# Kernel tuning notes

Hardware: AMD Instinct MI355X
Metric: run time of the kernel (lower is better)

Reference implementation:

```python
import jax, jax.numpy as jnp
import numpy as np

N, E = 40000, 640000
EMB, HID, H, TXT = 128, 128, 4, 384
C = HID // H  # per-head channels = 32


def _prelu(x, a):
    return jnp.where(x >= 0, x, a * x)


def _layernorm(x, g, b, eps=1e-5):
    m = jnp.mean(x, axis=-1, keepdims=True)
    v = jnp.mean((x - m) ** 2, axis=-1, keepdims=True)
    return (x - m) / jnp.sqrt(v + eps) * g + b


def _gat_conv(h, src, dst, W, att_src, att_dst, bias):
    # PyG GATConv (concat=True, eval mode): lin has no bias, self-loops already in src/dst.
    xh = (h @ W.T).reshape(N, H, C)                      # [N,H,C]
    a_src = jnp.sum(xh * att_src, axis=-1)               # [N,H]
    a_dst = jnp.sum(xh * att_dst, axis=-1)               # [N,H]
    alpha = jax.nn.leaky_relu(a_src[src] + a_dst[dst], negative_slope=0.2)  # [Et,H]
    amax = jax.ops.segment_max(alpha, dst, num_segments=N)
    ex = jnp.exp(alpha - amax[dst])
    denom = jax.ops.segment_sum(ex, dst, num_segments=N)
    coef = ex / denom[dst]                               # scatter-softmax over dst
    out = jax.ops.segment_sum(xh[src] * coef[:, :, None], dst, num_segments=N)
    return out.reshape(N, H * C) + bias


def setup_inputs() -> dict:
    key = jax.random.key(0)
    ks = jax.random.split(key, 20)
    nrm = lambda k, s, sc=0.05: jax.random.normal(k, s, jnp.float32) * sc
    inp = {
        "x": nrm(ks[0], (N, EMB), 1.0),
        "num_x": nrm(ks[1], (N, 1), 1.0),
        "num_mask": jnp.ones((N,), jnp.float32),
        "txt_x": nrm(ks[2], (N, TXT), 1.0),
        "txt_mask": jnp.ones((N,), jnp.float32),
        "edge_index": jax.random.randint(ks[3], (2, E), 0, N, jnp.int32),
        "num_proj_w": nrm(ks[4], (EMB, 1)), "num_proj_b": jnp.zeros((EMB,), jnp.float32),
        "txt_proj_w": nrm(ks[5], (EMB, TXT)), "txt_proj_b": jnp.zeros((EMB,), jnp.float32),
        "node_proj_w": nrm(ks[6], (HID, EMB)), "node_proj_b": jnp.zeros((HID,), jnp.float32),
        "prelu0_a": jnp.full((HID,), 0.25, jnp.float32),
        "conv1_w": nrm(ks[7], (HID, HID)), "att_src1": nrm(ks[8], (H, C)), "att_dst1": nrm(ks[9], (H, C)), "bias1": jnp.zeros((HID,), jnp.float32),
        "norm1_g": jnp.ones((HID,), jnp.float32), "norm1_b": jnp.zeros((HID,), jnp.float32),
        "prelu1_a": jnp.full((HID,), 0.25, jnp.float32),
        "conv2_w": nrm(ks[10], (HID, HID)), "att_src2": nrm(ks[11], (H, C)), "att_dst2": nrm(ks[12], (H, C)), "bias2": jnp.zeros((HID,), jnp.float32),
        "norm2_g": jnp.ones((HID,), jnp.float32), "norm2_b": jnp.zeros((HID,), jnp.float32),
        "prelu2_a": jnp.full((HID,), 0.25, jnp.float32),
        "out_w": nrm(ks[13], (1, HID)), "out_b": jnp.zeros((1,), jnp.float32),
    }
    return inp


def reference(x, num_x, num_mask, txt_x, txt_mask, edge_index,
              num_proj_w, num_proj_b, txt_proj_w, txt_proj_b,
              node_proj_w, node_proj_b, prelu0_a,
              conv1_w, att_src1, att_dst1, bias1, norm1_g, norm1_b, prelu1_a,
              conv2_w, att_src2, att_dst2, bias2, norm2_g, norm2_b, prelu2_a,
              out_w, out_b):
    # add self loops (PyG GATConv default)
    loop = jnp.arange(N, dtype=edge_index.dtype)
    src = jnp.concatenate([edge_index[0], loop])
    dst = jnp.concatenate([edge_index[1], loop])

    h = (num_x * num_mask[:, None]) @ num_proj_w.T + num_proj_b
    h = h + (txt_x * txt_mask[:, None]) @ txt_proj_w.T + txt_proj_b
    h = h + x @ node_proj_w.T + node_proj_b
    h = _prelu(h, prelu0_a)

    h = _gat_conv(h, src, dst, conv1_w, att_src1, att_dst1, bias1)
    h = _prelu(_layernorm(h, norm1_g, norm1_b), prelu1_a)  # dropout: eval mode -> identity

    h = _gat_conv(h, src, dst, conv2_w, att_src2, att_dst2, bias2)
    h = _prelu(_layernorm(h, norm2_g, norm2_b), prelu2_a)

    return (h @ out_w.T + out_b).squeeze(-1)  # [N]
```

## Files before the change

kernel.cpp:

```cpp
#include <hip/hip_runtime.h>
#include <stdint.h>

typedef unsigned short u16;
typedef unsigned int u32;
typedef __attribute__((ext_vector_type(8))) short bf16x8;
typedef __attribute__((ext_vector_type(4))) float f32x4;

__device__ __forceinline__ float bf2f(u32 u) {
    union { u32 i; float f; } v; v.i = u << 16; return v.f;
}
__device__ __forceinline__ u16 f2bf(float f) {
    u32 x = __float_as_uint(f);
    return (u16)((x + 0x7fffu + ((x >> 16) & 1u)) >> 16);
}
__device__ __forceinline__ float wred_sum(float v) {
#pragma unroll
    for (int o = 32; o > 0; o >>= 1) v += __shfl_xor(v, o, 64);
    return v;
}
__device__ __forceinline__ bf16x8 ldA_f32(const float* p, size_t off) {
    union { uint4 u; bf16x8 b; } t;
    const float* af = p + off;
    float4 a = *(const float4*)af, b2 = *(const float4*)(af + 4);
    t.u.x = (u32)f2bf(a.x)  | ((u32)f2bf(a.y)  << 16);
    t.u.y = (u32)f2bf(a.z)  | ((u32)f2bf(a.w)  << 16);
    t.u.z = (u32)f2bf(b2.x) | ((u32)f2bf(b2.y) << 16);
    t.u.w = (u32)f2bf(b2.z) | ((u32)f2bf(b2.w) << 16);
    return t.b;
}
__device__ __forceinline__ bf16x8 ld16B(const u16* p, size_t off) {
    union { uint4 u; bf16x8 b; } t; t.u = *(const uint4*)(p + off); return t.b;
}
__device__ __forceinline__ bf16x8 ldB(const u16* sw, int ct, int ks, int l16, int quad) {
    union { uint4 u; bf16x8 b; } t;
    t.u = *(const uint4*)&sw[(ct * 16 + l16) * 136 + ks * 32 + quad * 8];
    return t.b;
}
__device__ __forceinline__ void stage256_f32(const float* W, int stride, int koff,
                                             u16* sw, int tid) {
#pragma unroll
    for (int it = 0; it < 8; ++it) {
        int idx = (it * 256 + tid) * 8;
        int c = idx >> 7, kk = idx & 127;
        const float* wf = W + (size_t)c * stride + koff + kk;
        float4 a = *(const float4*)wf, b = *(const float4*)(wf + 4);
        uint4 v;
        v.x = (u32)f2bf(a.x) | ((u32)f2bf(a.y) << 16);
        v.y = (u32)f2bf(a.z) | ((u32)f2bf(a.w) << 16);
        v.z = (u32)f2bf(b.x) | ((u32)f2bf(b.y) << 16);
        v.w = (u32)f2bf(b.z) | ((u32)f2bf(b.w) << 16);
        *(uint4*)&sw[c * 136 + kk] = v;
    }
}

__global__ void k_zero(int* __restrict__ p, int n) {
    int i = blockIdx.x * 256 + threadIdx.x;
    if (i < n) p[i] = 0;
}
__global__ void k_hist(const int* __restrict__ dst, int E, int* __restrict__ deg) {
    int e = blockIdx.x * 256 + threadIdx.x;
    if (e < E) atomicAdd(&deg[dst[e]], 1);
}
__global__ __launch_bounds__(1024) void k_scanA(const int* __restrict__ deg, int n,
                                                int* __restrict__ out, int* __restrict__ bsum) {
    __shared__ int wsum[16];
    int t = threadIdx.x, w = t >> 6, lane = t & 63;
    int i0 = blockIdx.x * 4096 + t * 4;
    int4 v = make_int4(0, 0, 0, 0);
    if (i0 + 3 < n) v = *(const int4*)&deg[i0];
    else {
        if (i0 < n)     v.x = deg[i0];
        if (i0 + 1 < n) v.y = deg[i0 + 1];
        if (i0 + 2 < n) v.z = deg[i0 + 2];
    }
    int tsum = v.x + v.y + v.z + v.w;
    int s = tsum;
#pragma unroll
    for (int o = 1; o < 64; o <<= 1) { int u = __shfl_up(s, o, 64); if (lane >= o) s += u; }
    if (lane == 63) wsum[w] = s;
    __syncthreads();
    if (w == 0 && lane < 16) {
        int ws = wsum[lane];
#pragma unroll
        for (int o = 1; o < 16; o <<= 1) { int u = __shfl_up(ws, o, 64); if (lane >= o) ws += u; }
        wsum[lane] = ws;
    }
    __syncthreads();
    int woff = (w == 0) ? 0 : wsum[w - 1];
    int p = woff + s - tsum;
    if (i0 + 3 < n) {
        int4 o4; o4.x = p; o4.y = p + v.x; o4.z = p + v.x + v.y; o4.w = p + v.x + v.y + v.z;
        *(int4*)&out[i0] = o4;
    } else {
        int pp = p;
        if (i0 < n)     { out[i0] = pp;     pp += v.x; }
        if (i0 + 1 < n) { out[i0 + 1] = pp; pp += v.y; }
        if (i0 + 2 < n) { out[i0 + 2] = pp; }
    }
    if (t == 0) bsum[blockIdx.x] = wsum[15];
}
__global__ void k_scanB(int* __restrict__ bsum, int nb, int* __restrict__ total) {
    int lane = threadIdx.x;
    int v = (lane < nb) ? bsum[lane] : 0;
    int s = v;
#pragma unroll
    for (int o = 1; o < 64; o <<= 1) { int u = __shfl_up(s, o, 64); if (lane >= o) s += u; }
    if (lane < nb) bsum[lane] = s - v;
    if (lane == 63) total[0] = s;
}
__global__ void k_scanC(int* __restrict__ rowptr, int* __restrict__ cursor,
                        const int* __restrict__ boff, int n) {
    int i = blockIdx.x * 256 + threadIdx.x;
    if (i < n) {
        int r = rowptr[i] + boff[i >> 12];
        rowptr[i] = r; cursor[i] = r;
    }
}
__global__ void k_scatter(const int* __restrict__ srcp, const int* __restrict__ dstp, int E,
                          int* __restrict__ cursor, int* __restrict__ col) {
    int e = blockIdx.x * 256 + threadIdx.x;
    if (e < E) {
        int p = atomicAdd(&cursor[dstp[e]], 1);
        col[p] = srcp[e];
    }
}

__global__ __launch_bounds__(256) void k_inproj(
    const float* __restrict__ x, const float* __restrict__ numx, const float* __restrict__ numm,
    const float* __restrict__ txt, const float* __restrict__ txtm,
    const float* __restrict__ numw, const float* __restrict__ numb,
    const float* __restrict__ txtw, const float* __restrict__ txtb,
    const float* __restrict__ nodew, const float* __restrict__ nodeb,
    const float* __restrict__ pa, u16* __restrict__ h0) {
    __shared__ u16 sw[128 * 136];
    int tid = threadIdx.x;
    int w = tid >> 6, lane = tid & 63, quad = lane >> 4, l16 = lane & 15;
    int nb = blockIdx.x * 64 + w * 16;
    f32x4 acc[8];
#pragma unroll
    for (int ct = 0; ct < 8; ++ct) { f32x4 z = {0.f, 0.f, 0.f, 0.f}; acc[ct] = z; }

    for (int chunk = 0; chunk < 3; ++chunk) {
        __syncthreads();
        stage256_f32(txtw, 384, chunk * 128, sw, tid);
        __syncthreads();
#pragma unroll
        for (int ks = 0; ks < 4; ++ks) {
            bf16x8 a0 = ldA_f32(txt, (size_t)(nb + l16) * 384 + chunk * 128 + ks * 32 + quad * 8);
#pragma unroll
            for (int ct = 0; ct < 8; ++ct)
                acc[ct] = __builtin_amdgcn_mfma_f32_16x16x32_bf16(
                    a0, ldB(sw, ct, ks, l16, quad), acc[ct], 0, 0, 0);
        }
    }
#pragma unroll
    for (int r = 0; r < 4; ++r) {
        float tm = txtm[nb + quad * 4 + r];
#pragma unroll
        for (int ct = 0; ct < 8; ++ct) acc[ct][r] *= tm;
    }
    __syncthreads();
    stage256_f32(nodew, 128, 0, sw, tid);
    __syncthreads();
#pragma unroll
    for (int ks = 0; ks < 4; ++ks) {
        bf16x8 a0 = ldA_f32(x, (size_t)(nb + l16) * 128 + ks * 32 + quad * 8);
#pragma unroll
        for (int ct = 0; ct < 8; ++ct)
            acc[ct] = __builtin_amdgcn_mfma_f32_16x16x32_bf16(
                a0, ldB(sw, ct, ks, l16, quad), acc[ct], 0, 0, 0);
    }
    float nm[4];
#pragma unroll
    for (int r = 0; r < 4; ++r) {
        int n = nb + quad * 4 + r;
        nm[r] = numx[n] * numm[n];
    }
#pragma unroll
    for (int ct = 0; ct < 8; ++ct) {
        int c = ct * 16 + l16;
        float cw = numw[c];
        float cb = numb[c] + txtb[c] + nodeb[c];
        float pav = pa[c];
#pragma unroll
        for (int r = 0; r < 4; ++r) {
            int n = nb + quad * 4 + r;
            float v = acc[ct][r] + nm[r] * cw + cb;
            v = v >= 0.f ? v : pav * v;
            h0[(size_t)n * 128 + c] = f2bf(v);
        }
    }
}

__global__ __launch_bounds__(256) void k_xh(
    const u16* __restrict__ h, const float* __restrict__ W,
    const float* __restrict__ att_s, const float* __restrict__ att_d,
    u16* __restrict__ xh, float* __restrict__ asrc, float* __restrict__ adst) {
    __shared__ u16 sw[128 * 136];
    int tid = threadIdx.x;
    int w = tid >> 6, lane = tid & 63, quad = lane >> 4, l16 = lane & 15;
    int nb = blockIdx.x * 64 + w * 16;
    f32x4 acc[8];
#pragma unroll
    for (int ct = 0; ct < 8; ++ct) { f32x4 z = {0.f, 0.f, 0.f, 0.f}; acc[ct] = z; }

    stage256_f32(W, 128, 0, sw, tid);
    __syncthreads();
#pragma unroll
    for (int ks = 0; ks < 4; ++ks) {
        bf16x8 a0 = ld16B(h, (size_t)(nb + l16) * 128 + ks * 32 + quad * 8);
#pragma unroll
        for (int ct = 0; ct < 8; ++ct)
            acc[ct] = __builtin_amdgcn_mfma_f32_16x16x32_bf16(
                a0, ldB(sw, ct, ks, l16, quad), acc[ct], 0, 0, 0);
    }
#pragma unroll
    for (int ct = 0; ct < 8; ++ct) {
        int c = ct * 16 + l16;
#pragma unroll
        for (int r = 0; r < 4; ++r) {
            int n = nb + quad * 4 + r;
            xh[(size_t)n * 128 + c] = f2bf(acc[ct][r]);
        }
    }
    float as_[8], ad_[8];
#pragma unroll
    for (int ct = 0; ct < 8; ++ct) {
        int c = ct * 16 + l16;
        as_[ct] = att_s[c];
        ad_[ct] = att_d[c];
    }
#pragma unroll
    for (int hh = 0; hh < 4; ++hh) {
        float vs[4], vd[4];
#pragma unroll
        for (int r = 0; r < 4; ++r) {
            vs[r] = acc[2 * hh][r] * as_[2 * hh] + acc[2 * hh + 1][r] * as_[2 * hh + 1];
            vd[r] = acc[2 * hh][r] * ad_[2 * hh] + acc[2 * hh + 1][r] * ad_[2 * hh + 1];
        }
#pragma unroll
        for (int o = 1; o <= 8; o <<= 1) {
#pragma unroll
            for (int r = 0; r < 4; ++r) {
                vs[r] += __shfl_xor(vs[r], o, 64);
                vd[r] += __shfl_xor(vd[r], o, 64);
            }
        }
        if ((l16 >> 2) == hh) {
            int r = l16 & 3;
            float ss = (r == 0) ? vs[0] : (r == 1) ? vs[1] : (r == 2) ? vs[2] : vs[3];
            float dd = (r == 0) ? vd[0] : (r == 1) ? vd[1] : (r == 2) ? vd[2] : vd[3];
            int n = nb + quad * 4 + r;
            asrc[n * 4 + hh] = ss;
            adst[n * 4 + hh] = dd;
        }
    }
}

__global__ __launch_bounds__(64) void k_agg(
    const u16* __restrict__ xh, const float* __restrict__ asrc, const float* __restrict__ adst,
    const int* __restrict__ rowptr, const int* __restrict__ col,
    const float* __restrict__ bias, const float* __restrict__ g, const float* __restrict__ b,
    const float* __restrict__ pa, u16* __restrict__ hnext,
    const float* __restrict__ outw, const float* __restrict__ outb, float* __restrict__ outy,
    int is_final) {
    __shared__ int   scol[64];
    __shared__ float scoef[64][4];
    int n = blockIdx.x, lane = threadIdx.x;
    int beg = rowptr[n], end = rowptr[n + 1];
    const float4* asrc4 = (const float4*)asrc;

    float4 adv = ((const float4*)adst)[n];
    float ad[4] = { adv.x, adv.y, adv.z, adv.w };
    float4 asv = asrc4[n];
    float els[4];
    {
#pragma unroll
        for (int h = 0; h < 4; h++) {
            float a = ((const float*)&asv)[h] + ad[h];
            a = a >= 0.f ? a : 0.2f * a;
            els[h] = __expf(a);
        }
    }
    int hh = lane >> 4;
    u32 vself = ((const u32*)(xh + (size_t)n * 128))[lane];
    float acc0 = els[hh] * bf2f(vself & 0xffffu);
    float acc1 = els[hh] * bf2f(vself >> 16);
    float acc0b = 0.f, acc1b = 0.f;
    float l[4] = { 0.f, 0.f, 0.f, 0.f };

    for (int base = beg; base < end; base += 64) {
        int e = base + lane;
        int cnt = min(64, end - base);
        if (e < end) {
            int s = col[e];
            float4 av = asrc4[s];
            scol[lane] = s;
            float cf[4];
#pragma unroll
            for (int h = 0; h < 4; h++) {
                float a = ((const float*)&av)[h] + ad[h];
                a = a >= 0.f ? a : 0.2f * a;
                cf[h] = __expf(a);
                l[h] += cf[h];
            }
            *(float4*)scoef[lane] = make_float4(cf[0], cf[1], cf[2], cf[3]);
        }
        __syncthreads();
        int j = 0;
        for (; j + 1 < cnt; j += 2) {
            int s0 = scol[j], s1 = scol[j + 1];
            float c0 = scoef[j][hh], c1 = scoef[j + 1][hh];
            u32 v0 = ((const u32*)(xh + (size_t)s0 * 128))[lane];
            u32 v1 = ((const u32*)(xh + (size_t)s1 * 128))[lane];
            acc0  += c0 * bf2f(v0 & 0xffffu);
            acc1  += c0 * bf2f(v0 >> 16);
            acc0b += c1 * bf2f(v1 & 0xffffu);
            acc1b += c1 * bf2f(v1 >> 16);
        }
        if (j < cnt) {
            int s0 = scol[j];
            float c0 = scoef[j][hh];
            u32 v0 = ((const u32*)(xh + (size_t)s0 * 128))[lane];
            acc0 += c0 * bf2f(v0 & 0xffffu);
            acc1 += c0 * bf2f(v0 >> 16);
        }
        __syncthreads();
    }
    acc0 += acc0b;
    acc1 += acc1b;

    float L[4];
#pragma unroll
    for (int h = 0; h < 4; h++) L[h] = wred_sum(l[h]) + els[h];
    float inv = 1.f / L[hh];
    acc0 *= inv;
    acc1 *= inv;

    int c0i = 2 * lane;
    float2 bi = *(const float2*)(bias + c0i);
    acc0 += bi.x; acc1 += bi.y;

    float mean = wred_sum(acc0 + acc1) * (1.f / 128.f);
    float d0 = acc0 - mean, d1 = acc1 - mean;
    float var = wred_sum(d0 * d0 + d1 * d1) * (1.f / 128.f);
    float rstd = rsqrtf(var + 1e-5f);
    float2 gg = *(const float2*)(g + c0i);
    float2 bb = *(const float2*)(b + c0i);
    float2 pp = *(const float2*)(pa + c0i);
    float y0 = d0 * rstd * gg.x + bb.x;
    float y1 = d1 * rstd * gg.y + bb.y;
    y0 = y0 >= 0.f ? y0 : pp.x * y0;
    y1 = y1 >= 0.f ? y1 : pp.y * y1;

    if (is_final) {
        float2 ow = *(const float2*)(outw + c0i);
        float dot = wred_sum(y0 * ow.x + y1 * ow.y);
        if (lane == 0) outy[n] = dot + outb[0];
    } else {
        ((u32*)(hnext + (size_t)n * 128))[lane] = (u32)f2bf(y0) | ((u32)f2bf(y1) << 16);
    }
}

extern "C" void kernel_launch(void* const* d_in, const int* in_sizes, int n_in,
                              void* d_out, int out_size, void* d_ws, size_t ws_size,
                              hipStream_t stream) {
    const int N = in_sizes[2];
    const int E = in_sizes[5] / 2;

    const float* x      = (const float*)d_in[0];
    const float* numx   = (const float*)d_in[1];
    const float* numm   = (const float*)d_in[2];
    const float* txt    = (const float*)d_in[3];
    const float* txtm   = (const float*)d_in[4];
    const int*   ei     = (const int*)d_in[5];
    const float* numw   = (const float*)d_in[6];
    const float* numb   = (const float*)d_in[7];
    const float* txtw   = (const float*)d_in[8];
    const float* txtb   = (const float*)d_in[9];
    const float* nodew  = (const float*)d_in[10];
    const float* nodeb  = (const float*)d_in[11];
    const float* pa0    = (const float*)d_in[12];
    const float* conv1w = (const float*)d_in[13];
    const float* atts1  = (const float*)d_in[14];
    const float* attd1  = (const float*)d_in[15];
    const float* bias1  = (const float*)d_in[16];
    const float* g1     = (const float*)d_in[17];
    const float* b1     = (const float*)d_in[18];
    const float* pa1    = (const float*)d_in[19];
    const float* conv2w = (const float*)d_in[20];
    const float* atts2  = (const float*)d_in[21];
    const float* attd2  = (const float*)d_in[22];
    const float* bias2  = (const float*)d_in[23];
    const float* g2     = (const float*)d_in[24];
    const float* b2     = (const float*)d_in[25];
    const float* pa2    = (const float*)d_in[26];
    const float* outw   = (const float*)d_in[27];
    const float* outb   = (const float*)d_in[28];

    const int* srcp = ei;
    const int* dstp = ei + E;

    char* p = (char*)d_ws;
    auto alloc = [&](size_t bytes) -> void* {
        void* q = (void*)p;
        p += (bytes + 255) & ~(size_t)255;
        return q;
    };
    u16*   hA     = (u16*)alloc((size_t)N * 128 * 2);
    u16*   hB     = (u16*)alloc((size_t)N * 128 * 2);
    float* asrc   = (float*)alloc((size_t)N * 4 * 4);
    float* adst   = (float*)alloc((size_t)N * 4 * 4);
    int*   deg    = (int*)alloc((size_t)N * 4);
    int*   rowptr = (int*)alloc((size_t)(N + 1) * 4);
    int*   cursor = (int*)alloc((size_t)N * 4);
    int*   col    = (int*)alloc((size_t)E * 4);
    int*   bsum   = (int*)alloc(64 * 4);

    const int nbScan = (N + 4095) / 4096;
    k_zero<<<(N + 255) / 256, 256, 0, stream>>>(deg, N);
    k_hist<<<(E + 255) / 256, 256, 0, stream>>>(dstp, E, deg);
    k_scanA<<<nbScan, 1024, 0, stream>>>(deg, N, rowptr, bsum);
    k_scanB<<<1, 64, 0, stream>>>(bsum, nbScan, rowptr + N);
    k_scanC<<<(N + 255) / 256, 256, 0, stream>>>(rowptr, cursor, bsum, N);
    k_scatter<<<(E + 255) / 256, 256, 0, stream>>>(srcp, dstp, E, cursor, col);

    const int gProj = N / 64;

    k_inproj<<<gProj, 256, 0, stream>>>(x, numx, numm, txt, txtm, numw, numb,
                                        txtw, txtb, nodew, nodeb, pa0, hA);

    k_xh<<<gProj, 256, 0, stream>>>(hA, conv1w, atts1, attd1, hB, asrc, adst);
    k_agg<<<N, 64, 0, stream>>>(hB, asrc, adst, rowptr, col, bias1, g1, b1, pa1,
                                hA, nullptr, nullptr, nullptr, 0);

    k_xh<<<gProj, 256, 0, stream>>>(hA, conv2w, atts2, attd2, hB, asrc, adst);
    k_agg<<<N, 64, 0, stream>>>(hB, asrc, adst, rowptr, col, bias2, g2, b2, pa2,
                                nullptr, outw, outb, (float*)d_out, 1);
}
```

Before: 340.6 us.

## Fuse input projection with first GAT linear and unroll aggregation by four

The input projection kernel now keeps its PReLU output tile in shared memory and immediately runs the first GAT linear layer plus the attention-logit reductions. This removes the h0 round trip through global memory and one kernel launch. The edge aggregation loop is also unrolled to four neighbours with separate accumulators, so more gathers are in flight. The fused kernel uses more shared memory and registers, which may lower occupancy.

```diff
diff --git a/kernel.cpp b/kernel.cpp
--- a/kernel.cpp
+++ b/kernel.cpp
@@ -125,16 +125,18 @@
     }
 }
 
-__global__ __launch_bounds__(256) void k_inproj(
+__global__ __launch_bounds__(256) void k_fused1(
     const float* __restrict__ x, const float* __restrict__ numx, const float* __restrict__ numm,
     const float* __restrict__ txt, const float* __restrict__ txtm,
     const float* __restrict__ numw, const float* __restrict__ numb,
     const float* __restrict__ txtw, const float* __restrict__ txtb,
     const float* __restrict__ nodew, const float* __restrict__ nodeb,
-    const float* __restrict__ pa, u16* __restrict__ h0) {
+    const float* __restrict__ pa,
+    const float* __restrict__ W1, const float* __restrict__ atts, const float* __restrict__ attd,
+    u16* __restrict__ xh, float* __restrict__ asrc, float* __restrict__ adst) {
     __shared__ u16 sw[128 * 136];
-    int tid = threadIdx.x;
-    int w = tid >> 6, lane = tid & 63, quad = lane >> 4, l16 = lane & 15;
+    __shared__ u16 sh[4][16 * 136];
+    int tid = threadIdx.x, w = tid >> 6, lane = tid & 63, quad = lane >> 4, l16 = lane & 15;
     int nb = blockIdx.x * 64 + w * 16;
     f32x4 acc[8];
 #pragma unroll
@@ -184,10 +186,62 @@
         float pav = pa[c];
 #pragma unroll
         for (int r = 0; r < 4; ++r) {
-            int n = nb + quad * 4 + r;
             float v = acc[ct][r] + nm[r] * cw + cb;
             v = v >= 0.f ? v : pav * v;
-            h0[(size_t)n * 128 + c] = f2bf(v);
+            sh[w][(quad * 4 + r) * 136 + c] = f2bf(v);
+        }
+    }
+    __syncthreads();
+    stage256_f32(W1, 128, 0, sw, tid);
+    __syncthreads();
+    f32x4 a2[8];
+#pragma unroll
+    for (int ct = 0; ct < 8; ++ct) { f32x4 z = {0.f, 0.f, 0.f, 0.f}; a2[ct] = z; }
+#pragma unroll
+    for (int ks = 0; ks < 4; ++ks) {
+        bf16x8 a0 = ld16B(sh[w], l16 * 136 + ks * 32 + quad * 8);
+#pragma unroll
+        for (int ct = 0; ct < 8; ++ct)
+            a2[ct] = __builtin_amdgcn_mfma_f32_16x16x32_bf16(
+                a0, ldB(sw, ct, ks, l16, quad), a2[ct], 0, 0, 0);
+    }
+#pragma unroll
+    for (int ct = 0; ct < 8; ++ct) {
+        int c = ct * 16 + l16;
+#pragma unroll
+        for (int r = 0; r < 4; ++r)
+            xh[(size_t)(nb + quad * 4 + r) * 128 + c] = f2bf(a2[ct][r]);
+    }
+    float as_[8], ad_[8];
+#pragma unroll
+    for (int ct = 0; ct < 8; ++ct) {
+        int c = ct * 16 + l16;
+        as_[ct] = atts[c];
+        ad_[ct] = attd[c];
+    }
+#pragma unroll
+    for (int hh = 0; hh < 4; ++hh) {
+        float vs[4], vd[4];
+#pragma unroll
+        for (int r = 0; r < 4; ++r) {
+            vs[r] = a2[2 * hh][r] * as_[2 * hh] + a2[2 * hh + 1][r] * as_[2 * hh + 1];
+            vd[r] = a2[2 * hh][r] * ad_[2 * hh] + a2[2 * hh + 1][r] * ad_[2 * hh + 1];
+        }
+#pragma unroll
+        for (int o = 1; o <= 8; o <<= 1) {
+#pragma unroll
+            for (int r = 0; r < 4; ++r) {
+                vs[r] += __shfl_xor(vs[r], o, 64);
+                vd[r] += __shfl_xor(vd[r], o, 64);
+            }
+        }
+        if ((l16 >> 2) == hh) {
+            int r = l16 & 3;
+            float ss = (r == 0) ? vs[0] : (r == 1) ? vs[1] : (r == 2) ? vs[2] : vs[3];
+            float dd = (r == 0) ? vd[0] : (r == 1) ? vd[1] : (r == 2) ? vd[2] : vd[3];
+            int n = nb + quad * 4 + r;
+            asrc[n * 4 + hh] = ss;
+            adst[n * 4 + hh] = dd;
         }
     }
 }
@@ -274,19 +328,17 @@
     float ad[4] = { adv.x, adv.y, adv.z, adv.w };
     float4 asv = asrc4[n];
     float els[4];
-    {
-#pragma unroll
-        for (int h = 0; h < 4; h++) {
-            float a = ((const float*)&asv)[h] + ad[h];
-            a = a >= 0.f ? a : 0.2f * a;
-            els[h] = __expf(a);
-        }
+#pragma unroll
+    for (int h = 0; h < 4; h++) {
+        float a = ((const float*)&asv)[h] + ad[h];
+        a = a >= 0.f ? a : 0.2f * a;
+        els[h] = __expf(a);
     }
     int hh = lane >> 4;
     u32 vself = ((const u32*)(xh + (size_t)n * 128))[lane];
     float acc0 = els[hh] * bf2f(vself & 0xffffu);
     float acc1 = els[hh] * bf2f(vself >> 16);
-    float acc0b = 0.f, acc1b = 0.f;
+    float a0b = 0.f, a1b = 0.f, a0c = 0.f, a1c = 0.f, a0d = 0.f, a1d = 0.f;
     float l[4] = { 0.f, 0.f, 0.f, 0.f };
 
     for (int base = beg; base < end; base += 64) {
@@ -308,17 +360,20 @@
         }
         __syncthreads();
         int j = 0;
-        for (; j + 1 < cnt; j += 2) {
-            int s0 = scol[j], s1 = scol[j + 1];
+        for (; j + 3 < cnt; j += 4) {
+            int s0 = scol[j], s1 = scol[j + 1], s2 = scol[j + 2], s3 = scol[j + 3];
             float c0 = scoef[j][hh], c1 = scoef[j + 1][hh];
+            float c2 = scoef[j + 2][hh], c3 = scoef[j + 3][hh];
             u32 v0 = ((const u32*)(xh + (size_t)s0 * 128))[lane];
             u32 v1 = ((const u32*)(xh + (size_t)s1 * 128))[lane];
-            acc0  += c0 * bf2f(v0 & 0xffffu);
-            acc1  += c0 * bf2f(v0 >> 16);
-            acc0b += c1 * bf2f(v1 & 0xffffu);
-            acc1b += c1 * bf2f(v1 >> 16);
-        }
-        if (j < cnt) {
+            u32 v2 = ((const u32*)(xh + (size_t)s2 * 128))[lane];
+            u32 v3 = ((const u32*)(xh + (size_t)s3 * 128))[lane];
+            acc0 += c0 * bf2f(v0 & 0xffffu);  acc1 += c0 * bf2f(v0 >> 16);
+            a0b  += c1 * bf2f(v1 & 0xffffu);  a1b  += c1 * bf2f(v1 >> 16);
+            a0c  += c2 * bf2f(v2 & 0xffffu);  a1c  += c2 * bf2f(v2 >> 16);
+            a0d  += c3 * bf2f(v3 & 0xffffu);  a1d  += c3 * bf2f(v3 >> 16);
+        }
+        for (; j < cnt; ++j) {
             int s0 = scol[j];
             float c0 = scoef[j][hh];
             u32 v0 = ((const u32*)(xh + (size_t)s0 * 128))[lane];
@@ -327,8 +382,8 @@
         }
         __syncthreads();
     }
-    acc0 += acc0b;
-    acc1 += acc1b;
+    acc0 += a0b + a0c + a0d;
+    acc1 += a1b + a1c + a1d;
 
     float L[4];
 #pragma unroll
@@ -427,10 +482,9 @@
 
     const int gProj = N / 64;
 
-    k_inproj<<<gProj, 256, 0, stream>>>(x, numx, numm, txt, txtm, numw, numb,
-                                        txtw, txtb, nodew, nodeb, pa0, hA);
-
-    k_xh<<<gProj, 256, 0, stream>>>(hA, conv1w, atts1, attd1, hB, asrc, adst);
+    k_fused1<<<gProj, 256, 0, stream>>>(x, numx, numm, txt, txtm, numw, numb,
+                                        txtw, txtb, nodew, nodeb, pa0,
+                                        conv1w, atts1, attd1, hB, asrc, adst);
     k_agg<<<N, 64, 0, stream>>>(hB, asrc, adst, rowptr, col, bias1, g1, b1, pa1,
                                 hA, nullptr, nullptr, nullptr, 0);
 
```

Measured after the change: 330.4 us. -3.0%, faster.
